# Kernel optimization log

Measured on AMD Instinct MI355X. Metric: run time of the kernel, lower is better.

The kernel has to match this reference:

```python
import jax, jax.numpy as jnp
import numpy as np

IN_CH = 128
OUT_CH = 1
N_NODES = 20000
N_EDGES = 640000
EPS = 1e-5


def setup_inputs() -> dict:
    key = jax.random.key(0)
    ks = jax.random.split(key, 8)
    x = jax.random.normal(ks[0], (N_NODES, IN_CH), dtype=jnp.float32)
    edge_index = jax.random.randint(ks[1], (2, N_EDGES), 0, N_NODES, dtype=jnp.int64)
    s1 = 1.0 / np.sqrt(2 * IN_CH)
    s2 = 1.0 / np.sqrt(IN_CH)
    return {
        "x": x,
        "edge_index": edge_index,
        "W1": jax.random.normal(ks[2], (2 * IN_CH, IN_CH), dtype=jnp.float32) * s1,
        "b1": jnp.zeros((IN_CH,), dtype=jnp.float32),
        "bn_g": jnp.ones((IN_CH,), dtype=jnp.float32),
        "bn_b": jnp.zeros((IN_CH,), dtype=jnp.float32),
        "W2": jax.random.normal(ks[3], (IN_CH, IN_CH), dtype=jnp.float32) * s2,
        "b2": jnp.zeros((IN_CH,), dtype=jnp.float32),
        "ln_g": jnp.ones((IN_CH,), dtype=jnp.float32),
        "ln_b": jnp.zeros((IN_CH,), dtype=jnp.float32),
        "W3": jax.random.normal(ks[4], (IN_CH, OUT_CH), dtype=jnp.float32) * s2,
        "b3": jnp.zeros((OUT_CH,), dtype=jnp.float32),
    }


def gcn_conv(h, src, dst, num_nodes, bias):
    # h: [num_nodes, F] already linearly transformed. GCN norm with self loops:
    # deg[i] = 1 + in-degree(i); norm_e = deg[src]^-1/2 * deg[dst]^-1/2
    deg = jnp.zeros((num_nodes,), h.dtype).at[dst].add(1.0) + 1.0
    dinv = deg ** -0.5
    norm = dinv[src] * dinv[dst]                      # [E]
    agg = jnp.zeros_like(h).at[dst].add(h[src] * norm[:, None])
    agg = agg + h * (dinv * dinv)[:, None]            # self-loop contribution
    return agg + bias


def reference(x, edge_index, W1, b1, bn_g, bn_b, W2, b2, ln_g, ln_b, W3, b3):
    src, dst = edge_index[0], edge_index[1]
    E = src.shape[0]
    # edge features: [E, 2*IN_CH]
    ef = jnp.concatenate([x[src], x[dst]], axis=1)
    # GCNConv 1 over E "nodes" (edge-feature rows)
    h = gcn_conv(ef @ W1, src, dst, E, b1)
    # BatchNorm1d (training-mode batch stats, biased variance)
    mean = h.mean(axis=0)
    var = h.var(axis=0)
    h = (h - mean) * jax.lax.rsqrt(var + EPS) * bn_g + bn_b
    h = jax.nn.relu(h)
    # GCNConv 2
    h = gcn_conv(h @ W2, src, dst, E, b2)
    # LayerNorm over feature dim
    mu = h.mean(axis=-1, keepdims=True)
    v = h.var(axis=-1, keepdims=True)
    h = (h - mu) * jax.lax.rsqrt(v + EPS) * ln_g + ln_b
    h = jax.nn.relu(h)
    out = h @ W3 + b3                                  # [E, 1]
    return out.squeeze()
```

## Files before the change

### kernel.cpp

```cpp
#include <hip/hip_runtime.h>
#include <hip/hip_bf16.h>

#define NN 20000
#define NE 640000
#define TAILN (NE - NN)
#define F  128
#define EPSN 1e-5f

typedef __bf16 bf16;
typedef bf16  bf16x8 __attribute__((ext_vector_type(8)));
typedef bf16  bf16x4 __attribute__((ext_vector_type(4)));
typedef float f32x4  __attribute__((ext_vector_type(4)));
typedef float f32x2  __attribute__((ext_vector_type(2)));
typedef unsigned short u16;

__global__ void k_cvt_idx(const void* __restrict__ ei_raw, int* __restrict__ srcb,
                          int* __restrict__ dstb, int* __restrict__ cnt,
                          int* __restrict__ cst, int* __restrict__ cdt) {
  const int* e32 = (const int*)ei_raw;
  const long long* e64 = (const long long*)ei_raw;
  bool is64 = true;
#pragma unroll
  for (int k = 0; k < 8; ++k) is64 = is64 && (e32[2 * k + 1] == 0);
  int e = blockIdx.x * 256 + threadIdx.x;
  if (e < NE) {
    int s, d;
    if (is64) { s = (int)e64[e]; d = (int)e64[NE + e]; }
    else      { s = e32[e];      d = e32[NE + e]; }
    srcb[e] = s; dstb[e] = d;
    atomicAdd(&cnt[d], 1);
    if (e >= NN) { atomicAdd(&cst[s], 1); atomicAdd(&cdt[d], 1); }
  }
}

__global__ __launch_bounds__(256) void k1_gemm1(const float* __restrict__ x,
        const float* __restrict__ W1, bf16* __restrict__ xa, bf16* __restrict__ xb) {
  __shared__ float XT[64][129];
  int row0 = blockIdx.x * 64;
  int half = blockIdx.y >> 1;
  int cb   = (blockIdx.y & 1) * 64;
  const float* W = W1 + (size_t)half * F * F;
  bf16* out = half ? xb : xa;
  int t = threadIdx.x;
#pragma unroll
  for (int i = 0; i < 8; ++i) {
    int flat = i * 1024 + t * 4;
    int r = flat >> 7, c = flat & 127;
    int gr = row0 + r;
    f32x4 v = {0.f, 0.f, 0.f, 0.f};
    if (gr < NN) v = *(const f32x4*)(x + (size_t)gr * F + c);
    XT[r][c] = v[0]; XT[r][c + 1] = v[1]; XT[r][c + 2] = v[2]; XT[r][c + 3] = v[3];
  }
  __syncthreads();
  int tc = t & 15, tr = t >> 4;
  float acc[4][4] = {};
  for (int k = 0; k < F; ++k) {
    f32x4 wv = *(const f32x4*)(W + (size_t)k * F + cb + tc * 4);
    float x0 = XT[tr * 4 + 0][k], x1 = XT[tr * 4 + 1][k];
    float x2 = XT[tr * 4 + 2][k], x3 = XT[tr * 4 + 3][k];
#pragma unroll
    for (int j = 0; j < 4; ++j) {
      acc[0][j] += x0 * wv[j]; acc[1][j] += x1 * wv[j];
      acc[2][j] += x2 * wv[j]; acc[3][j] += x3 * wv[j];
    }
  }
#pragma unroll
  for (int i = 0; i < 4; ++i) {
    int gr = row0 + tr * 4 + i;
    if (gr < NN) {
      bf16x4 o;
#pragma unroll
      for (int j = 0; j < 4; ++j) o[j] = (bf16)acc[i][j];
      *(bf16x4*)(out + (size_t)gr * F + cb + tc * 4) = o;
    }
  }
}

__global__ __launch_bounds__(1024) void k3_scan(const int* __restrict__ cnt,
        int* __restrict__ ptr, int* __restrict__ cursor,
        float* __restrict__ dinv, float* __restrict__ invdeg) {
  __shared__ int wsum[16];
  __shared__ int carry_s;
  int t = threadIdx.x;
  int lane = t & 63, wv = t >> 6;
  if (t == 0) carry_s = 0;
  __syncthreads();
  for (int c0 = 0; c0 < NN; c0 += 1024) {
    int i = c0 + t;
    int v = (i < NN) ? cnt[i] : 0;
    int s = v;
#pragma unroll
    for (int off = 1; off < 64; off <<= 1) {
      int n = __shfl_up(s, off);
      if (lane >= off) s += n;
    }
    if (lane == 63) wsum[wv] = s;
    __syncthreads();
    int carry = carry_s;
    int wbase = 0;
#pragma unroll
    for (int k2 = 0; k2 < 16; ++k2) wbase += (k2 < wv) ? wsum[k2] : 0;
    int incl = s + wbase;
    if (i < NN) {
      int excl = carry + incl - v;
      ptr[i] = excl; cursor[i] = excl;
      float deg = (float)(v + 1);
      dinv[i] = rsqrtf(deg);
      invdeg[i] = 1.0f / deg;
    }
    __syncthreads();
    if (t == 1023) carry_s = carry + incl;
    __syncthreads();
  }
  if (t == 0) ptr[NN] = carry_s;
}

__global__ void k4_hhead(const int* __restrict__ srcb, const int* __restrict__ dstb,
                         const bf16* __restrict__ xa, const bf16* __restrict__ xb,
                         bf16* __restrict__ hh) {
  int flat = blockIdx.x * 256 + threadIdx.x;
  int j = flat >> 4, ch = flat & 15;
  if (j >= NN) return;
  int s = srcb[j], d = dstb[j];
  bf16x8 a = *(const bf16x8*)(xa + (size_t)s * F + ch * 8);
  bf16x8 b = *(const bf16x8*)(xb + (size_t)d * F + ch * 8);
  bf16x8 o;
#pragma unroll
  for (int m = 0; m < 8; ++m) o[m] = (bf16)((float)a[m] + (float)b[m]);
  *(bf16x8*)(hh + (size_t)j * F + ch * 8) = o;
}

__global__ void k5_fill(const int* __restrict__ srcb, const int* __restrict__ dstb,
                        int* __restrict__ cursor, int* __restrict__ csr_s) {
  int e = blockIdx.x * 256 + threadIdx.x;
  if (e < NE) {
    int d = dstb[e];
    int pos = atomicAdd(&cursor[d], 1);
    csr_s[pos] = srcb[e] | ((e >= NN) ? (1 << 16) : 0);
  }
}

__global__ __launch_bounds__(256) void k6_conv1cross(const int* __restrict__ ptr,
        const int* __restrict__ csr_s, const bf16* __restrict__ hh,
        const bf16* __restrict__ xa, const bf16* __restrict__ xb,
        const float* __restrict__ dinv, const float* __restrict__ invdeg,
        const float* __restrict__ b1, float* __restrict__ h1h,
        float* __restrict__ crossrow) {
  int w = threadIdx.x >> 6, lane = threadIdx.x & 63;
  int g = lane >> 4, k = lane & 15;
  int i = blockIdx.x * 4 + w;
  int c0 = k * 8;
  int beg = ptr[i], end = ptr[i + 1];
  float acc[8] = {0,0,0,0,0,0,0,0}, z[8] = {0,0,0,0,0,0,0,0};
  int q = beg + g;
  for (; q + 4 < end; q += 8) {
    int v0 = csr_s[q], v1 = csr_s[q + 4];
    int s0 = v0 & 0xFFFF, s1 = v1 & 0xFFFF;
    float f0 = (v0 >> 16) ? 1.f : 0.f, f1 = (v1 >> 16) ? 1.f : 0.f;
    float d0 = dinv[s0], d1 = dinv[s1];
    bf16x8 h0 = *(const bf16x8*)(hh + (size_t)s0 * F + c0);
    bf16x8 x0 = *(const bf16x8*)(xa + (size_t)s0 * F + c0);
    bf16x8 h1 = *(const bf16x8*)(hh + (size_t)s1 * F + c0);
    bf16x8 x1 = *(const bf16x8*)(xa + (size_t)s1 * F + c0);
#pragma unroll
    for (int j = 0; j < 8; ++j) {
      acc[j] += d0 * (float)h0[j] + d1 * (float)h1[j];
      z[j]   += f0 * (float)x0[j] + f1 * (float)x1[j];
    }
  }
  if (q < end) {
    int v0 = csr_s[q];
    int s0 = v0 & 0xFFFF;
    float f0 = (v0 >> 16) ? 1.f : 0.f;
    float d0 = dinv[s0];
    bf16x8 h0 = *(const bf16x8*)(hh + (size_t)s0 * F + c0);
    bf16x8 x0 = *(const bf16x8*)(xa + (size_t)s0 * F + c0);
#pragma unroll
    for (int j = 0; j < 8; ++j) {
      acc[j] += d0 * (float)h0[j];
      z[j]   += f0 * (float)x0[j];
    }
  }
#pragma unroll
  for (int m = 16; m < 64; m <<= 1) {
#pragma unroll
    for (int j = 0; j < 8; ++j) {
      acc[j] += __shfl_xor(acc[j], m);
      z[j]   += __shfl_xor(z[j], m);
    }
  }
  if (g == 0) {
    float di = dinv[i], iv = invdeg[i];
    bf16x8 self = *(const bf16x8*)(hh + (size_t)i * F + c0);
    f32x4 bA = *(const f32x4*)(b1 + c0), bB = *(const f32x4*)(b1 + c0 + 4);
    f32x4 o0, o1;
#pragma unroll
    for (int j = 0; j < 4; ++j) {
      o0[j] = di * acc[j]     + (float)self[j]     * iv + bA[j];
      o1[j] = di * acc[j + 4] + (float)self[j + 4] * iv + bB[j];
    }
    *(f32x4*)(h1h + (size_t)i * F + c0) = o0;
    *(f32x4*)(h1h + (size_t)i * F + c0 + 4) = o1;
  } else if (g == 1) {
    bf16x8 xbv = *(const bf16x8*)(xb + (size_t)i * F + c0);
    f32x4 o0, o1;
#pragma unroll
    for (int j = 0; j < 4; ++j) {
      o0[j] = (float)xbv[j]     * z[j];
      o1[j] = (float)xbv[j + 4] * z[j + 4];
    }
    *(f32x4*)(crossrow + (size_t)i * F + c0) = o0;
    *(f32x4*)(crossrow + (size_t)i * F + c0 + 4) = o1;
  }
}

__global__ __launch_bounds__(256) void k7sr(const float* __restrict__ h1h,
        const float* __restrict__ crossrow, const bf16* __restrict__ xa,
        const bf16* __restrict__ xb, const int* __restrict__ cst,
        const int* __restrict__ cdt, float* __restrict__ statsB) {
  int t = threadIdx.x;
  int w = t >> 6, lane = t & 63, k = lane & 15;
  int rg = t >> 4;
  int c0 = k * 8;
  int base = blockIdx.x * 200;
  float A1[8] = {0,0,0,0,0,0,0,0}, A2[8] = {0,0,0,0,0,0,0,0};
  float B1[8] = {0,0,0,0,0,0,0,0}, B2[8] = {0,0,0,0,0,0,0,0};
  float Cc[8] = {0,0,0,0,0,0,0,0};
  for (int r = rg; r < 200; r += 16) {
    int n = base + r;
    f32x4 h0 = *(const f32x4*)(h1h + (size_t)n * F + c0);
    f32x4 h1 = *(const f32x4*)(h1h + (size_t)n * F + c0 + 4);
    f32x4 cr0 = *(const f32x4*)(crossrow + (size_t)n * F + c0);
    f32x4 cr1 = *(const f32x4*)(crossrow + (size_t)n * F + c0 + 4);
    bf16x8 av = *(const bf16x8*)(xa + (size_t)n * F + c0);
    bf16x8 bv = *(const bf16x8*)(xb + (size_t)n * F + c0);
    float ca = (float)cst[n], cb = (float)cdt[n];
#pragma unroll
    for (int j = 0; j < 4; ++j) {
      A1[j] += h0[j]; A2[j] += h0[j] * h0[j];
      A1[j + 4] += h1[j]; A2[j + 4] += h1[j] * h1[j];
      Cc[j] += cr0[j]; Cc[j + 4] += cr1[j];
    }
#pragma unroll
    for (int j = 0; j < 8; ++j) {
      float a = (float)av[j], b = (float)bv[j];
      B1[j] += ca * a + cb * b;
      B2[j] += ca * a * a + cb * b * b;
    }
  }
#pragma unroll
  for (int m = 16; m < 64; m <<= 1) {
#pragma unroll
    for (int j = 0; j < 8; ++j) {
      A1[j] += __shfl_xor(A1[j], m); A2[j] += __shfl_xor(A2[j], m);
      B1[j] += __shfl_xor(B1[j], m); B2[j] += __shfl_xor(B2[j], m);
      Cc[j] += __shfl_xor(Cc[j], m);
    }
  }
  __shared__ float L[4][5][128];
  if (lane < 16) {
#pragma unroll
    for (int j = 0; j < 8; ++j) {
      L[w][0][c0 + j] = A1[j]; L[w][1][c0 + j] = A2[j];
      L[w][2][c0 + j] = B1[j]; L[w][3][c0 + j] = B2[j];
      L[w][4][c0 + j] = Cc[j];
    }
  }
  __syncthreads();
  if (t < 128) {
#pragma unroll
    for (int term = 0; term < 5; ++term) {
      float v = L[0][term][t] + L[1][term][t] + L[2][term][t] + L[3][term][t];
      atomicAdd(&statsB[term * 128 + t], v);
    }
  }
}

__global__ __launch_bounds__(256) void k8_final(const float* __restrict__ statsB,
        const float* __restrict__ bn_g, const float* __restrict__ bn_b,
        const float* __restrict__ b1, const float* __restrict__ W2,
        const float* __restrict__ b2, const float* __restrict__ lng,
        const float* __restrict__ lnb, const float* __restrict__ W3,
        float* __restrict__ P, float* __restrict__ Qh, float* __restrict__ Qt,
        u16* __restrict__ W2t, f32x4* __restrict__ params4) {
  int t = threadIdx.x;
  if (t < 128) {
    float A1 = statsB[t], A2 = statsB[128 + t], B1v = statsB[256 + t];
    float B2v = statsB[384 + t], Cv = statsB[512 + t];
    float b1c = b1[t];
    float S = A1 + B1v + (float)TAILN * b1c;
    float Q = A2 + B2v + 2.f * Cv + 2.f * b1c * B1v + (float)TAILN * b1c * b1c;
    float mean = S * (1.0f / NE);
    float var = Q * (1.0f / NE) - mean * mean;
    float rs = rsqrtf(var + EPSN);
    float p = bn_g[t] * rs;
    float sh = bn_b[t] - mean * p;
    P[t] = p; Qh[t] = sh; Qt[t] = p * b1c + sh;
    f32x4 pr = {b2[t], lng[t], lnb[t], W3[t]};
    params4[t] = pr;
  }
  for (int i = 0; i < 64; ++i) {
    int flat = i * 256 + t;
    int k = flat >> 7, c = flat & 127;
    union { bf16 b; u16 u; } cv;
    cv.b = (bf16)W2[(size_t)k * F + c];
    W2t[(size_t)c * F + k] = cv.u;
  }
}

__global__ __launch_bounds__(256) void k9a_headgemm(const float* __restrict__ h1h,
        const float* __restrict__ P, const float* __restrict__ Qh,
        const u16* __restrict__ W2t, bf16* __restrict__ h2ph) {
  __shared__ __align__(16) bf16 A[64 * 128];
  __shared__ __align__(16) bf16 B[128 * 128];
  int t = threadIdx.x;
  int row0 = blockIdx.x * 64;
  const bf16x8* srcB = (const bf16x8*)W2t;
#pragma unroll
  for (int i = 0; i < 8; ++i) {
    int ch = i * 256 + t;
    int r = ch >> 4, cir = ch & 15;
    *(bf16x8*)&B[r * 128 + ((cir ^ (r & 7)) << 3)] = srcB[ch];
  }
  {
    int r = t >> 2, sub = t & 3;
    int gr = row0 + r;
#pragma unroll
    for (int j = 0; j < 4; ++j) {
      int c0 = sub * 32 + j * 8;
      f32x4 v0 = {0.f,0.f,0.f,0.f}, v1 = {0.f,0.f,0.f,0.f};
      if (gr < NN) {
        v0 = *(const f32x4*)(h1h + (size_t)gr * F + c0);
        v1 = *(const f32x4*)(h1h + (size_t)gr * F + c0 + 4);
      }
      f32x4 p0 = *(const f32x4*)(P + c0), p1 = *(const f32x4*)(P + c0 + 4);
      f32x4 q0 = *(const f32x4*)(Qh + c0), q1 = *(const f32x4*)(Qh + c0 + 4);
      bf16x8 o;
#pragma unroll
      for (int m = 0; m < 4; ++m) {
        o[m]     = (bf16)fmaxf(v0[m] * p0[m] + q0[m], 0.f);
        o[m + 4] = (bf16)fmaxf(v1[m] * p1[m] + q1[m], 0.f);
      }
      int ch = c0 >> 3;
      *(bf16x8*)&A[r * 128 + ((ch ^ (r & 7)) << 3)] = o;
    }
  }
  __syncthreads();
  int lane = t & 63, w = t >> 6;
  int lr = lane & 15, g = lane >> 4;
  int arow = w * 16 + lr;
  bf16x8 af[4];
#pragma unroll
  for (int kk = 0; kk < 4; ++kk)
    af[kk] = *(const bf16x8*)&A[arow * 128 + (((kk * 4 + g) ^ (arow & 7)) << 3)];
  f32x4 acc[8];
#pragma unroll
  for (int n = 0; n < 8; ++n) {
    f32x4 a = {0.f,0.f,0.f,0.f};
    int col = n * 16 + lr;
#pragma unroll
    for (int kk = 0; kk < 4; ++kk) {
      bf16x8 bfr = *(const bf16x8*)&B[col * 128 + (((kk * 4 + g) ^ (col & 7)) << 3)];
      a = __builtin_amdgcn_mfma_f32_16x16x32_bf16(af[kk], bfr, a, 0, 0, 0);
    }
    acc[n] = a;
  }
#pragma unroll
  for (int n = 0; n < 8; ++n) {
#pragma unroll
    for (int r4 = 0; r4 < 4; ++r4) {
      int gr = row0 + w * 16 + g * 4 + r4;
      if (gr < NN) h2ph[(size_t)gr * F + n * 16 + lr] = (bf16)acc[n][r4];
    }
  }
}

__global__ __launch_bounds__(256) void k9b_head(const int* __restrict__ ptr,
        const int* __restrict__ csr_s, const bf16* __restrict__ h2ph,
        const float* __restrict__ dinv, const float* __restrict__ invdeg,
        const float* __restrict__ b2, const float* __restrict__ lng,
        const float* __restrict__ lnb, const float* __restrict__ W3,
        const float* __restrict__ b3, float* __restrict__ out) {
  int w = threadIdx.x >> 6, lane = threadIdx.x & 63;
  int g = lane >> 4, k = lane & 15;
  int i = blockIdx.x * 4 + w;
  int c0 = k * 8;
  int beg = ptr[i], end = ptr[i + 1];
  float acc[8] = {0,0,0,0,0,0,0,0};
  int q = beg + g;
  for (; q + 4 < end; q += 8) {
    int s0 = csr_s[q] & 0xFFFF, s1 = csr_s[q + 4] & 0xFFFF;
    float d0 = dinv[s0], d1 = dinv[s1];
    bf16x8 h0 = *(const bf16x8*)(h2ph + (size_t)s0 * F + c0);
    bf16x8 h1 = *(const bf16x8*)(h2ph + (size_t)s1 * F + c0);
#pragma unroll
    for (int j = 0; j < 8; ++j)
      acc[j] += d0 * (float)h0[j] + d1 * (float)h1[j];
  }
  if (q < end) {
    int s0 = csr_s[q] & 0xFFFF;
    float d0 = dinv[s0];
    bf16x8 h0 = *(const bf16x8*)(h2ph + (size_t)s0 * F + c0);
#pragma unroll
    for (int j = 0; j < 8; ++j) acc[j] += d0 * (float)h0[j];
  }
#pragma unroll
  for (int m = 16; m < 64; m <<= 1) {
#pragma unroll
    for (int j = 0; j < 8; ++j) acc[j] += __shfl_xor(acc[j], m);
  }
  float di = dinv[i], iv = invdeg[i];
  bf16x8 self = *(const bf16x8*)(h2ph + (size_t)i * F + c0);
  f32x4 b2A = *(const f32x4*)(b2 + c0), b2B = *(const f32x4*)(b2 + c0 + 4);
  float h2[8];
#pragma unroll
  for (int j = 0; j < 4; ++j) {
    h2[j]     = di * acc[j]     + (float)self[j]     * iv + b2A[j];
    h2[j + 4] = di * acc[j + 4] + (float)self[j + 4] * iv + b2B[j];
  }
  float s1v = 0.f, s2v = 0.f;
#pragma unroll
  for (int j = 0; j < 8; ++j) { s1v += h2[j]; s2v += h2[j] * h2[j]; }
#pragma unroll
  for (int m = 1; m < 16; m <<= 1) { s1v += __shfl_xor(s1v, m); s2v += __shfl_xor(s2v, m); }
  float mean = s1v * (1.0f / F);
  float var = s2v * (1.0f / F) - mean * mean;
  float rs = rsqrtf(var + EPSN);
  f32x4 lgA = *(const f32x4*)(lng + c0), lgB = *(const f32x4*)(lng + c0 + 4);
  f32x4 lbA = *(const f32x4*)(lnb + c0), lbB = *(const f32x4*)(lnb + c0 + 4);
  f32x4 w3A = *(const f32x4*)(W3 + c0),  w3B = *(const f32x4*)(W3 + c0 + 4);
  float y = 0.f;
#pragma unroll
  for (int j = 0; j < 4; ++j) {
    y += fmaxf((h2[j]     - mean) * rs * lgA[j] + lbA[j], 0.f) * w3A[j];
    y += fmaxf((h2[j + 4] - mean) * rs * lgB[j] + lbB[j], 0.f) * w3B[j];
  }
#pragma unroll
  for (int m = 1; m < 16; m <<= 1) y += __shfl_xor(y, m);
  if (lane == 0) out[i] = y + b3[0];
}

__global__ __launch_bounds__(256) void k9c_tail(const int* __restrict__ srcb,
        const int* __restrict__ dstb, const bf16* __restrict__ xa,
        const bf16* __restrict__ xb, const float* __restrict__ P,
        const float* __restrict__ Qt, const u16* __restrict__ W2t,
        const f32x4* __restrict__ params4, const float* __restrict__ b3,
        float* __restrict__ out) {
  __shared__ __align__(16) bf16 B[128 * 128];
  int t = threadIdx.x;
  const bf16x8* srcB = (const bf16x8*)W2t;
#pragma unroll
  for (int i = 0; i < 8; ++i) {
    int ch = i * 256 + t;
    int r = ch >> 4, cir = ch & 15;
    *(bf16x8*)&B[r * 128 + ((cir ^ (r & 7)) << 3)] = srcB[ch];
  }
  __syncthreads();
  int lane = t & 63, w = t >> 6;
  int lr = lane & 15, g = lane >> 4;
  int ebase = NN + blockIdx.x * 256 + w * 64;
  float b3v = b3[0];
  for (int rc = 0; rc < 4; ++rc) {
    int e = ebase + rc * 16 + lr;
    bool ok = (e < NE);
    int se = 0, de = 0;
    if (ok) { se = srcb[e]; de = dstb[e]; }
    bf16x8 af[4];
#pragma unroll
    for (int kk = 0; kk < 4; ++kk) {
      int c0 = kk * 32 + g * 8;
      bf16x8 o;
      if (ok) {
        bf16x8 av = *(const bf16x8*)(xa + (size_t)se * F + c0);
        bf16x8 bv = *(const bf16x8*)(xb + (size_t)de * F + c0);
        f32x4 p0 = *(const f32x4*)(P + c0), p1 = *(const f32x4*)(P + c0 + 4);
        f32x4 q0 = *(const f32x4*)(Qt + c0), q1 = *(const f32x4*)(Qt + c0 + 4);
#pragma unroll
        for (int m = 0; m < 4; ++m) {
          o[m]     = (bf16)fmaxf(((float)av[m] + (float)bv[m]) * p0[m] + q0[m], 0.f);
          o[m + 4] = (bf16)fmaxf(((float)av[m + 4] + (float)bv[m + 4]) * p1[m] + q1[m], 0.f);
        }
      } else {
#pragma unroll
        for (int m = 0; m < 8; ++m) o[m] = (bf16)0.f;
      }
      af[kk] = o;
    }
    f32x4 acc[8];
#pragma unroll
    for (int n = 0; n < 8; ++n) {
      f32x4 a = {0.f,0.f,0.f,0.f};
      int col = n * 16 + lr;
#pragma unroll
      for (int kk = 0; kk < 4; ++kk) {
        bf16x8 bfr = *(const bf16x8*)&B[col * 128 + (((kk * 4 + g) ^ (col & 7)) << 3)];
        a = __builtin_amdgcn_mfma_f32_16x16x32_bf16(af[kk], bfr, a, 0, 0, 0);
      }
      acc[n] = a;
    }
#pragma unroll
    for (int r4 = 0; r4 < 4; ++r4) {
      float vv[8];
      float s = 0.f, q = 0.f;
#pragma unroll
      for (int n = 0; n < 8; ++n) {
        float v = acc[n][r4] + params4[n * 16 + lr][0];
        vv[n] = v; s += v; q += v * v;
      }
#pragma unroll
      for (int m = 1; m < 16; m <<= 1) { s += __shfl_xor(s, m); q += __shfl_xor(q, m); }
      float mean = s * (1.0f / F);
      float var = q * (1.0f / F) - mean * mean;
      float rs = rsqrtf(var + EPSN);
      float o = 0.f;
#pragma unroll
      for (int n = 0; n < 8; ++n) {
        f32x4 pr = params4[n * 16 + lr];
        o += fmaxf((vv[n] - mean) * rs * pr[1] + pr[2], 0.f) * pr[3];
      }
#pragma unroll
      for (int m = 1; m < 16; m <<= 1) o += __shfl_xor(o, m);
      int eo = ebase + rc * 16 + g * 4 + r4;
      if (lr == 0 && eo < NE) out[eo] = o + b3v;
    }
  }
}

extern "C" void kernel_launch(void* const* d_in, const int* in_sizes, int n_in,
                              void* d_out, int out_size, void* d_ws, size_t ws_size,
                              hipStream_t stream) {
  const float* x   = (const float*)d_in[0];
  const void*  ei  = d_in[1];
  const float* W1  = (const float*)d_in[2];
  const float* b1  = (const float*)d_in[3];
  const float* bng = (const float*)d_in[4];
  const float* bnb = (const float*)d_in[5];
  const float* W2  = (const float*)d_in[6];
  const float* b2  = (const float*)d_in[7];
  const float* lng = (const float*)d_in[8];
  const float* lnb = (const float*)d_in[9];
  const float* W3  = (const float*)d_in[10];
  const float* b3  = (const float*)d_in[11];
  float* out = (float*)d_out;

  char* ws = (char*)d_ws;
  size_t off = 0;
  auto alloc = [&](size_t bytes) -> char* {
    off = (off + 511) & ~(size_t)511;
    char* p = ws + off;
    off += bytes;
    return p;
  };
  const size_t NFh = (size_t)NN * F * 2;
  bf16*  xa     = (bf16*)alloc(NFh);
  bf16*  xb     = (bf16*)alloc(NFh);
  bf16*  hh     = (bf16*)alloc(NFh);
  float* h1h    = (float*)alloc((size_t)NN * F * 4);
  float* crossr = (float*)alloc((size_t)NN * F * 4);
  int*   srcb   = (int*)alloc((size_t)NE * 4);
  int*   dstb   = (int*)alloc((size_t)NE * 4);
  int*   csr_s  = (int*)alloc((size_t)NE * 4);
  int*   cnt    = (int*)alloc((size_t)NN * 4);
  int*   cst    = (int*)alloc((size_t)NN * 4);
  int*   cdt    = (int*)alloc((size_t)NN * 4);
  int*   ptrb   = (int*)alloc((size_t)(NN + 1) * 4);
  int*   cursor = (int*)alloc((size_t)NN * 4);
  float* dinv   = (float*)alloc((size_t)NN * 4);
  float* invdeg = (float*)alloc((size_t)NN * 4);
  float* statsB = (float*)alloc(5 * 128 * 4);
  float* Pp     = (float*)alloc(128 * 4);
  float* Qh     = (float*)alloc(128 * 4);
  float* Qt     = (float*)alloc(128 * 4);
  u16*   W2t    = (u16*)alloc((size_t)F * F * 2);
  f32x4* params4= (f32x4*)alloc(128 * 16);
  bf16*  h2ph   = hh;

  hipMemsetAsync(cnt, 0, (size_t)NN * 4, stream);
  hipMemsetAsync(cst, 0, (size_t)NN * 4, stream);
  hipMemsetAsync(cdt, 0, (size_t)NN * 4, stream);
  hipMemsetAsync(statsB, 0, 5 * 128 * 4, stream);

  k_cvt_idx<<<2500, 256, 0, stream>>>(ei, srcb, dstb, cnt, cst, cdt);
  k1_gemm1<<<dim3(313, 4), 256, 0, stream>>>(x, W1, xa, xb);
  k3_scan<<<1, 1024, 0, stream>>>(cnt, ptrb, cursor, dinv, invdeg);
  k4_hhead<<<1250, 256, 0, stream>>>(srcb, dstb, xa, xb, hh);
  k5_fill<<<2500, 256, 0, stream>>>(srcb, dstb, cursor, csr_s);
  k6_conv1cross<<<5000, 256, 0, stream>>>(ptrb, csr_s, hh, xa, xb, dinv, invdeg, b1,
                                          h1h, crossr);
  k7sr<<<100, 256, 0, stream>>>(h1h, crossr, xa, xb, cst, cdt, statsB);
  k8_final<<<1, 256, 0, stream>>>(statsB, bng, bnb, b1, W2, b2, lng, lnb, W3,
                                  Pp, Qh, Qt, W2t, params4);
  k9a_headgemm<<<313, 256, 0, stream>>>(h1h, Pp, Qh, W2t, h2ph);
  k9b_head<<<5000, 256, 0, stream>>>(ptrb, csr_s, h2ph, dinv, invdeg, b2, lng, lnb,
                                     W3, b3, out);
  k9c_tail<<<2422, 256, 0, stream>>>(srcb, dstb, xa, xb, Pp, Qt, W2t, params4,
                                     b3, out);
}
```

Baseline: 461.0 us.

## Merge independent kernels into block-range fused launches to cut launch count

Independent kernels are merged into single launches that branch on block index: index conversion with the first GEMM and W2 transpose/param packing, head-sum with CSR fill, and the head and tail output kernels. The W2 transpose moves out of the single-block k8 into the first fused kernel, leaving k8 as a 128-thread stats finalize. This removes several launch gaps and tail-drain serialisation between kernels. In exchange the fused kernels carry the larger shared-memory footprint and register pressure of their heaviest branch, which can lower occupancy for the light branches, especially the 32KB LDS tile in kC applied to head blocks.

```diff
diff --git a/kernel.cpp b/kernel.cpp
--- a/kernel.cpp
+++ b/kernel.cpp
@@ -11,67 +11,86 @@
 typedef bf16  bf16x8 __attribute__((ext_vector_type(8)));
 typedef bf16  bf16x4 __attribute__((ext_vector_type(4)));
 typedef float f32x4  __attribute__((ext_vector_type(4)));
-typedef float f32x2  __attribute__((ext_vector_type(2)));
 typedef unsigned short u16;
 
-__global__ void k_cvt_idx(const void* __restrict__ ei_raw, int* __restrict__ srcb,
-                          int* __restrict__ dstb, int* __restrict__ cnt,
-                          int* __restrict__ cst, int* __restrict__ cdt) {
-  const int* e32 = (const int*)ei_raw;
-  const long long* e64 = (const long long*)ei_raw;
-  bool is64 = true;
-#pragma unroll
-  for (int k = 0; k < 8; ++k) is64 = is64 && (e32[2 * k + 1] == 0);
-  int e = blockIdx.x * 256 + threadIdx.x;
-  if (e < NE) {
-    int s, d;
-    if (is64) { s = (int)e64[e]; d = (int)e64[NE + e]; }
-    else      { s = e32[e];      d = e32[NE + e]; }
-    srcb[e] = s; dstb[e] = d;
-    atomicAdd(&cnt[d], 1);
-    if (e >= NN) { atomicAdd(&cst[s], 1); atomicAdd(&cdt[d], 1); }
-  }
-}
-
-__global__ __launch_bounds__(256) void k1_gemm1(const float* __restrict__ x,
-        const float* __restrict__ W1, bf16* __restrict__ xa, bf16* __restrict__ xb) {
+__global__ __launch_bounds__(256) void kA_fused(const void* __restrict__ ei_raw,
+        int* __restrict__ srcb, int* __restrict__ dstb, int* __restrict__ cnt,
+        int* __restrict__ cst, int* __restrict__ cdt,
+        const float* __restrict__ x, const float* __restrict__ W1,
+        bf16* __restrict__ xa, bf16* __restrict__ xb,
+        const float* __restrict__ W2, const float* __restrict__ b2,
+        const float* __restrict__ lng, const float* __restrict__ lnb,
+        const float* __restrict__ W3, u16* __restrict__ W2t,
+        f32x4* __restrict__ params4) {
   __shared__ float XT[64][129];
-  int row0 = blockIdx.x * 64;
-  int half = blockIdx.y >> 1;
-  int cb   = (blockIdx.y & 1) * 64;
-  const float* W = W1 + (size_t)half * F * F;
-  bf16* out = half ? xb : xa;
+  int bid = blockIdx.x;
   int t = threadIdx.x;
-#pragma unroll
-  for (int i = 0; i < 8; ++i) {
-    int flat = i * 1024 + t * 4;
-    int r = flat >> 7, c = flat & 127;
-    int gr = row0 + r;
-    f32x4 v = {0.f, 0.f, 0.f, 0.f};
-    if (gr < NN) v = *(const f32x4*)(x + (size_t)gr * F + c);
-    XT[r][c] = v[0]; XT[r][c + 1] = v[1]; XT[r][c + 2] = v[2]; XT[r][c + 3] = v[3];
-  }
-  __syncthreads();
-  int tc = t & 15, tr = t >> 4;
-  float acc[4][4] = {};
-  for (int k = 0; k < F; ++k) {
-    f32x4 wv = *(const f32x4*)(W + (size_t)k * F + cb + tc * 4);
-    float x0 = XT[tr * 4 + 0][k], x1 = XT[tr * 4 + 1][k];
-    float x2 = XT[tr * 4 + 2][k], x3 = XT[tr * 4 + 3][k];
-#pragma unroll
-    for (int j = 0; j < 4; ++j) {
-      acc[0][j] += x0 * wv[j]; acc[1][j] += x1 * wv[j];
-      acc[2][j] += x2 * wv[j]; acc[3][j] += x3 * wv[j];
-    }
-  }
-#pragma unroll
-  for (int i = 0; i < 4; ++i) {
-    int gr = row0 + tr * 4 + i;
-    if (gr < NN) {
-      bf16x4 o;
-#pragma unroll
-      for (int j = 0; j < 4; ++j) o[j] = (bf16)acc[i][j];
-      *(bf16x4*)(out + (size_t)gr * F + cb + tc * 4) = o;
+  if (bid < 2500) {
+    const int* e32 = (const int*)ei_raw;
+    const long long* e64 = (const long long*)ei_raw;
+    bool is64 = true;
+#pragma unroll
+    for (int k = 0; k < 8; ++k) is64 = is64 && (e32[2 * k + 1] == 0);
+    int e = bid * 256 + t;
+    if (e < NE) {
+      int s, d;
+      if (is64) { s = (int)e64[e]; d = (int)e64[NE + e]; }
+      else      { s = e32[e];      d = e32[NE + e]; }
+      srcb[e] = s; dstb[e] = d;
+      atomicAdd(&cnt[d], 1);
+      if (e >= NN) { atomicAdd(&cst[s], 1); atomicAdd(&cdt[d], 1); }
+    }
+  } else if (bid < 3752) {
+    int idx = bid - 2500;
+    int row0 = (idx >> 2) * 64;
+    int by = idx & 3;
+    int half = by >> 1;
+    int cb = (by & 1) * 64;
+    const float* W = W1 + (size_t)half * F * F;
+    bf16* out = half ? xb : xa;
+#pragma unroll
+    for (int i = 0; i < 8; ++i) {
+      int flat = i * 1024 + t * 4;
+      int r = flat >> 7, c = flat & 127;
+      int gr = row0 + r;
+      f32x4 v = {0.f, 0.f, 0.f, 0.f};
+      if (gr < NN) v = *(const f32x4*)(x + (size_t)gr * F + c);
+      XT[r][c] = v[0]; XT[r][c + 1] = v[1]; XT[r][c + 2] = v[2]; XT[r][c + 3] = v[3];
+    }
+    __syncthreads();
+    int tc = t & 15, tr = t >> 4;
+    float acc[4][4] = {};
+    for (int k = 0; k < F; ++k) {
+      f32x4 wv = *(const f32x4*)(W + (size_t)k * F + cb + tc * 4);
+      float x0 = XT[tr * 4 + 0][k], x1 = XT[tr * 4 + 1][k];
+      float x2 = XT[tr * 4 + 2][k], x3 = XT[tr * 4 + 3][k];
+#pragma unroll
+      for (int j = 0; j < 4; ++j) {
+        acc[0][j] += x0 * wv[j]; acc[1][j] += x1 * wv[j];
+        acc[2][j] += x2 * wv[j]; acc[3][j] += x3 * wv[j];
+      }
+    }
+#pragma unroll
+    for (int i = 0; i < 4; ++i) {
+      int gr = row0 + tr * 4 + i;
+      if (gr < NN) {
+        bf16x4 o;
+#pragma unroll
+        for (int j = 0; j < 4; ++j) o[j] = (bf16)acc[i][j];
+        *(bf16x4*)(out + (size_t)gr * F + cb + tc * 4) = o;
+      }
+    }
+  } else {
+    if (t < 128) {
+      f32x4 pr = {b2[t], lng[t], lnb[t], W3[t]};
+      params4[t] = pr;
+    }
+    for (int i = 0; i < 64; ++i) {
+      int flat = i * 256 + t;
+      int k = flat >> 7, c = flat & 127;
+      union { bf16 b; u16 u; } cv;
+      cv.b = (bf16)W2[(size_t)k * F + c];
+      W2t[(size_t)c * F + k] = cv.u;
     }
   }
 }
@@ -115,28 +134,30 @@
   if (t == 0) ptr[NN] = carry_s;
 }
 
-__global__ void k4_hhead(const int* __restrict__ srcb, const int* __restrict__ dstb,
-                         const bf16* __restrict__ xa, const bf16* __restrict__ xb,
-                         bf16* __restrict__ hh) {
-  int flat = blockIdx.x * 256 + threadIdx.x;
-  int j = flat >> 4, ch = flat & 15;
-  if (j >= NN) return;
-  int s = srcb[j], d = dstb[j];
-  bf16x8 a = *(const bf16x8*)(xa + (size_t)s * F + ch * 8);
-  bf16x8 b = *(const bf16x8*)(xb + (size_t)d * F + ch * 8);
-  bf16x8 o;
-#pragma unroll
-  for (int m = 0; m < 8; ++m) o[m] = (bf16)((float)a[m] + (float)b[m]);
-  *(bf16x8*)(hh + (size_t)j * F + ch * 8) = o;
-}
-
-__global__ void k5_fill(const int* __restrict__ srcb, const int* __restrict__ dstb,
-                        int* __restrict__ cursor, int* __restrict__ csr_s) {
-  int e = blockIdx.x * 256 + threadIdx.x;
-  if (e < NE) {
-    int d = dstb[e];
-    int pos = atomicAdd(&cursor[d], 1);
-    csr_s[pos] = srcb[e] | ((e >= NN) ? (1 << 16) : 0);
+__global__ __launch_bounds__(256) void kB_fused(const int* __restrict__ srcb,
+        const int* __restrict__ dstb, const bf16* __restrict__ xa,
+        const bf16* __restrict__ xb, bf16* __restrict__ hh,
+        int* __restrict__ cursor, int* __restrict__ csr_s) {
+  int bid = blockIdx.x;
+  int t = threadIdx.x;
+  if (bid < 1250) {
+    int flat = bid * 256 + t;
+    int j = flat >> 4, ch = flat & 15;
+    if (j >= NN) return;
+    int s = srcb[j], d = dstb[j];
+    bf16x8 a = *(const bf16x8*)(xa + (size_t)s * F + ch * 8);
+    bf16x8 b = *(const bf16x8*)(xb + (size_t)d * F + ch * 8);
+    bf16x8 o;
+#pragma unroll
+    for (int m = 0; m < 8; ++m) o[m] = (bf16)((float)a[m] + (float)b[m]);
+    *(bf16x8*)(hh + (size_t)j * F + ch * 8) = o;
+  } else {
+    int e = (bid - 1250) * 256 + t;
+    if (e < NE) {
+      int d = dstb[e];
+      int pos = atomicAdd(&cursor[d], 1);
+      csr_s[pos] = srcb[e] | ((e >= NN) ? (1 << 16) : 0);
+    }
   }
 }
 
@@ -276,36 +297,22 @@
   }
 }
 
-__global__ __launch_bounds__(256) void k8_final(const float* __restrict__ statsB,
+__global__ __launch_bounds__(128) void k8_small(const float* __restrict__ statsB,
         const float* __restrict__ bn_g, const float* __restrict__ bn_b,
-        const float* __restrict__ b1, const float* __restrict__ W2,
-        const float* __restrict__ b2, const float* __restrict__ lng,
-        const float* __restrict__ lnb, const float* __restrict__ W3,
-        float* __restrict__ P, float* __restrict__ Qh, float* __restrict__ Qt,
-        u16* __restrict__ W2t, f32x4* __restrict__ params4) {
+        const float* __restrict__ b1,
+        float* __restrict__ P, float* __restrict__ Qh, float* __restrict__ Qt) {
   int t = threadIdx.x;
-  if (t < 128) {
-    float A1 = statsB[t], A2 = statsB[128 + t], B1v = statsB[256 + t];
-    float B2v = statsB[384 + t], Cv = statsB[512 + t];
-    float b1c = b1[t];
-    float S = A1 + B1v + (float)TAILN * b1c;
-    float Q = A2 + B2v + 2.f * Cv + 2.f * b1c * B1v + (float)TAILN * b1c * b1c;
-    float mean = S * (1.0f / NE);
-    float var = Q * (1.0f / NE) - mean * mean;
-    float rs = rsqrtf(var + EPSN);
-    float p = bn_g[t] * rs;
-    float sh = bn_b[t] - mean * p;
-    P[t] = p; Qh[t] = sh; Qt[t] = p * b1c + sh;
-    f32x4 pr = {b2[t], lng[t], lnb[t], W3[t]};
-    params4[t] = pr;
-  }
-  for (int i = 0; i < 64; ++i) {
-    int flat = i * 256 + t;
-    int k = flat >> 7, c = flat & 127;
-    union { bf16 b; u16 u; } cv;
-    cv.b = (bf16)W2[(size_t)k * F + c];
-    W2t[(size_t)c * F + k] = cv.u;
-  }
+  float A1 = statsB[t], A2 = statsB[128 + t], B1v = statsB[256 + t];
+  float B2v = statsB[384 + t], Cv = statsB[512 + t];
+  float b1c = b1[t];
+  float S = A1 + B1v + (float)TAILN * b1c;
+  float Q = A2 + B2v + 2.f * Cv + 2.f * b1c * B1v + (float)TAILN * b1c * b1c;
+  float mean = S * (1.0f / NE);
+  float var = Q * (1.0f / NE) - mean * mean;
+  float rs = rsqrtf(var + EPSN);
+  float p = bn_g[t] * rs;
+  float sh = bn_b[t] - mean * p;
+  P[t] = p; Qh[t] = sh; Qt[t] = p * b1c + sh;
 }
 
 __global__ __launch_bounds__(256) void k9a_headgemm(const float* __restrict__ h1h,
@@ -375,153 +382,153 @@
   }
 }
 
-__global__ __launch_bounds__(256) void k9b_head(const int* __restrict__ ptr,
+__global__ __launch_bounds__(256) void kC_fused(const int* __restrict__ ptr,
         const int* __restrict__ csr_s, const bf16* __restrict__ h2ph,
         const float* __restrict__ dinv, const float* __restrict__ invdeg,
         const float* __restrict__ b2, const float* __restrict__ lng,
         const float* __restrict__ lnb, const float* __restrict__ W3,
-        const float* __restrict__ b3, float* __restrict__ out) {
-  int w = threadIdx.x >> 6, lane = threadIdx.x & 63;
-  int g = lane >> 4, k = lane & 15;
-  int i = blockIdx.x * 4 + w;
-  int c0 = k * 8;
-  int beg = ptr[i], end = ptr[i + 1];
-  float acc[8] = {0,0,0,0,0,0,0,0};
-  int q = beg + g;
-  for (; q + 4 < end; q += 8) {
-    int s0 = csr_s[q] & 0xFFFF, s1 = csr_s[q + 4] & 0xFFFF;
-    float d0 = dinv[s0], d1 = dinv[s1];
-    bf16x8 h0 = *(const bf16x8*)(h2ph + (size_t)s0 * F + c0);
-    bf16x8 h1 = *(const bf16x8*)(h2ph + (size_t)s1 * F + c0);
-#pragma unroll
-    for (int j = 0; j < 8; ++j)
-      acc[j] += d0 * (float)h0[j] + d1 * (float)h1[j];
-  }
-  if (q < end) {
-    int s0 = csr_s[q] & 0xFFFF;
-    float d0 = dinv[s0];
-    bf16x8 h0 = *(const bf16x8*)(h2ph + (size_t)s0 * F + c0);
-#pragma unroll
-    for (int j = 0; j < 8; ++j) acc[j] += d0 * (float)h0[j];
-  }
-#pragma unroll
-  for (int m = 16; m < 64; m <<= 1) {
-#pragma unroll
-    for (int j = 0; j < 8; ++j) acc[j] += __shfl_xor(acc[j], m);
-  }
-  float di = dinv[i], iv = invdeg[i];
-  bf16x8 self = *(const bf16x8*)(h2ph + (size_t)i * F + c0);
-  f32x4 b2A = *(const f32x4*)(b2 + c0), b2B = *(const f32x4*)(b2 + c0 + 4);
-  float h2[8];
-#pragma unroll
-  for (int j = 0; j < 4; ++j) {
-    h2[j]     = di * acc[j]     + (float)self[j]     * iv + b2A[j];
-    h2[j + 4] = di * acc[j + 4] + (float)self[j + 4] * iv + b2B[j];
-  }
-  float s1v = 0.f, s2v = 0.f;
-#pragma unroll
-  for (int j = 0; j < 8; ++j) { s1v += h2[j]; s2v += h2[j] * h2[j]; }
-#pragma unroll
-  for (int m = 1; m < 16; m <<= 1) { s1v += __shfl_xor(s1v, m); s2v += __shfl_xor(s2v, m); }
-  float mean = s1v * (1.0f / F);
-  float var = s2v * (1.0f / F) - mean * mean;
-  float rs = rsqrtf(var + EPSN);
-  f32x4 lgA = *(const f32x4*)(lng + c0), lgB = *(const f32x4*)(lng + c0 + 4);
-  f32x4 lbA = *(const f32x4*)(lnb + c0), lbB = *(const f32x4*)(lnb + c0 + 4);
-  f32x4 w3A = *(const f32x4*)(W3 + c0),  w3B = *(const f32x4*)(W3 + c0 + 4);
-  float y = 0.f;
-#pragma unroll
-  for (int j = 0; j < 4; ++j) {
-    y += fmaxf((h2[j]     - mean) * rs * lgA[j] + lbA[j], 0.f) * w3A[j];
-    y += fmaxf((h2[j + 4] - mean) * rs * lgB[j] + lbB[j], 0.f) * w3B[j];
-  }
-#pragma unroll
-  for (int m = 1; m < 16; m <<= 1) y += __shfl_xor(y, m);
-  if (lane == 0) out[i] = y + b3[0];
-}
-
-__global__ __launch_bounds__(256) void k9c_tail(const int* __restrict__ srcb,
-        const int* __restrict__ dstb, const bf16* __restrict__ xa,
-        const bf16* __restrict__ xb, const float* __restrict__ P,
-        const float* __restrict__ Qt, const u16* __restrict__ W2t,
-        const f32x4* __restrict__ params4, const float* __restrict__ b3,
-        float* __restrict__ out) {
+        const float* __restrict__ b3, float* __restrict__ out,
+        const int* __restrict__ srcb, const int* __restrict__ dstb,
+        const bf16* __restrict__ xa, const bf16* __restrict__ xb,
+        const float* __restrict__ P, const float* __restrict__ Qt,
+        const u16* __restrict__ W2t, const f32x4* __restrict__ params4) {
   __shared__ __align__(16) bf16 B[128 * 128];
+  int bid = blockIdx.x;
   int t = threadIdx.x;
-  const bf16x8* srcB = (const bf16x8*)W2t;
-#pragma unroll
-  for (int i = 0; i < 8; ++i) {
-    int ch = i * 256 + t;
-    int r = ch >> 4, cir = ch & 15;
-    *(bf16x8*)&B[r * 128 + ((cir ^ (r & 7)) << 3)] = srcB[ch];
-  }
-  __syncthreads();
   int lane = t & 63, w = t >> 6;
-  int lr = lane & 15, g = lane >> 4;
-  int ebase = NN + blockIdx.x * 256 + w * 64;
-  float b3v = b3[0];
-  for (int rc = 0; rc < 4; ++rc) {
-    int e = ebase + rc * 16 + lr;
-    bool ok = (e < NE);
-    int se = 0, de = 0;
-    if (ok) { se = srcb[e]; de = dstb[e]; }
-    bf16x8 af[4];
-#pragma unroll
-    for (int kk = 0; kk < 4; ++kk) {
-      int c0 = kk * 32 + g * 8;
-      bf16x8 o;
-      if (ok) {
-        bf16x8 av = *(const bf16x8*)(xa + (size_t)se * F + c0);
-        bf16x8 bv = *(const bf16x8*)(xb + (size_t)de * F + c0);
-        f32x4 p0 = *(const f32x4*)(P + c0), p1 = *(const f32x4*)(P + c0 + 4);
-        f32x4 q0 = *(const f32x4*)(Qt + c0), q1 = *(const f32x4*)(Qt + c0 + 4);
-#pragma unroll
-        for (int m = 0; m < 4; ++m) {
-          o[m]     = (bf16)fmaxf(((float)av[m] + (float)bv[m]) * p0[m] + q0[m], 0.f);
-          o[m + 4] = (bf16)fmaxf(((float)av[m + 4] + (float)bv[m + 4]) * p1[m] + q1[m], 0.f);
+  if (bid < 5000) {
+    int g = lane >> 4, k = lane & 15;
+    int i = bid * 4 + w;
+    int c0 = k * 8;
+    int beg = ptr[i], end = ptr[i + 1];
+    float acc[8] = {0,0,0,0,0,0,0,0};
+    int q = beg + g;
+    for (; q + 4 < end; q += 8) {
+      int s0 = csr_s[q] & 0xFFFF, s1 = csr_s[q + 4] & 0xFFFF;
+      float d0 = dinv[s0], d1 = dinv[s1];
+      bf16x8 h0 = *(const bf16x8*)(h2ph + (size_t)s0 * F + c0);
+      bf16x8 h1 = *(const bf16x8*)(h2ph + (size_t)s1 * F + c0);
+#pragma unroll
+      for (int j = 0; j < 8; ++j)
+        acc[j] += d0 * (float)h0[j] + d1 * (float)h1[j];
+    }
+    if (q < end) {
+      int s0 = csr_s[q] & 0xFFFF;
+      float d0 = dinv[s0];
+      bf16x8 h0 = *(const bf16x8*)(h2ph + (size_t)s0 * F + c0);
+#pragma unroll
+      for (int j = 0; j < 8; ++j) acc[j] += d0 * (float)h0[j];
+    }
+#pragma unroll
+    for (int m = 16; m < 64; m <<= 1) {
+#pragma unroll
+      for (int j = 0; j < 8; ++j) acc[j] += __shfl_xor(acc[j], m);
+    }
+    float di = dinv[i], iv = invdeg[i];
+    bf16x8 self = *(const bf16x8*)(h2ph + (size_t)i * F + c0);
+    f32x4 b2A = *(const f32x4*)(b2 + c0), b2B = *(const f32x4*)(b2 + c0 + 4);
+    float h2[8];
+#pragma unroll
+    for (int j = 0; j < 4; ++j) {
+      h2[j]     = di * acc[j]     + (float)self[j]     * iv + b2A[j];
+      h2[j + 4] = di * acc[j + 4] + (float)self[j + 4] * iv + b2B[j];
+    }
+    float s1v = 0.f, s2v = 0.f;
+#pragma unroll
+    for (int j = 0; j < 8; ++j) { s1v += h2[j]; s2v += h2[j] * h2[j]; }
+#pragma unroll
+    for (int m = 1; m < 16; m <<= 1) { s1v += __shfl_xor(s1v, m); s2v += __shfl_xor(s2v, m); }
+    float mean = s1v * (1.0f / F);
+    float var = s2v * (1.0f / F) - mean * mean;
+    float rs = rsqrtf(var + EPSN);
+    f32x4 lgA = *(const f32x4*)(lng + c0), lgB = *(const f32x4*)(lng + c0 + 4);
+    f32x4 lbA = *(const f32x4*)(lnb + c0), lbB = *(const f32x4*)(lnb + c0 + 4);
+    f32x4 w3A = *(const f32x4*)(W3 + c0),  w3B = *(const f32x4*)(W3 + c0 + 4);
+    float y = 0.f;
+#pragma unroll
+    for (int j = 0; j < 4; ++j) {
+      y += fmaxf((h2[j]     - mean) * rs * lgA[j] + lbA[j], 0.f) * w3A[j];
+      y += fmaxf((h2[j + 4] - mean) * rs * lgB[j] + lbB[j], 0.f) * w3B[j];
+    }
+#pragma unroll
+    for (int m = 1; m < 16; m <<= 1) y += __shfl_xor(y, m);
+    if (lane == 0) out[i] = y + b3[0];
+  } else {
+    int bid2 = bid - 5000;
+    const bf16x8* srcB = (const bf16x8*)W2t;
+#pragma unroll
+    for (int i = 0; i < 8; ++i) {
+      int ch = i * 256 + t;
+      int r = ch >> 4, cir = ch & 15;
+      *(bf16x8*)&B[r * 128 + ((cir ^ (r & 7)) << 3)] = srcB[ch];
+    }
+    __syncthreads();
+    int lr = lane & 15, g = lane >> 4;
+    int ebase = NN + bid2 * 256 + w * 64;
+    float b3v = b3[0];
+    for (int rc = 0; rc < 4; ++rc) {
+      int e = ebase + rc * 16 + lr;
+      bool ok = (e < NE);
+      int se = 0, de = 0;
+      if (ok) { se = srcb[e]; de = dstb[e]; }
+      bf16x8 af[4];
+#pragma unroll
+      for (int kk = 0; kk < 4; ++kk) {
+        int c0 = kk * 32 + g * 8;
+        bf16x8 o;
+        if (ok) {
+          bf16x8 av = *(const bf16x8*)(xa + (size_t)se * F + c0);
+          bf16x8 bv = *(const bf16x8*)(xb + (size_t)de * F + c0);
+          f32x4 p0 = *(const f32x4*)(P + c0), p1 = *(const f32x4*)(P + c0 + 4);
+          f32x4 q0 = *(const f32x4*)(Qt + c0), q1 = *(const f32x4*)(Qt + c0 + 4);
+#pragma unroll
+          for (int m = 0; m < 4; ++m) {
+            o[m]     = (bf16)fmaxf(((float)av[m] + (float)bv[m]) * p0[m] + q0[m], 0.f);
+            o[m + 4] = (bf16)fmaxf(((float)av[m + 4] + (float)bv[m + 4]) * p1[m] + q1[m], 0.f);
+          }
+        } else {
+#pragma unroll
+          for (int m = 0; m < 8; ++m) o[m] = (bf16)0.f;
         }
-      } else {
-#pragma unroll
-        for (int m = 0; m < 8; ++m) o[m] = (bf16)0.f;
+        af[kk] = o;
       }
-      af[kk] = o;
-    }
-    f32x4 acc[8];
-#pragma unroll
-    for (int n = 0; n < 8; ++n) {
-      f32x4 a = {0.f,0.f,0.f,0.f};
-      int col = n * 16 + lr;
-#pragma unroll
-      for (int kk = 0; kk < 4; ++kk) {
-        bf16x8 bfr = *(const bf16x8*)&B[col * 128 + (((kk * 4 + g) ^ (col & 7)) << 3)];
-        a = __builtin_amdgcn_mfma_f32_16x16x32_bf16(af[kk], bfr, a, 0, 0, 0);
+      f32x4 acc[8];
+#pragma unroll
+      for (int n = 0; n < 8; ++n) {
+        f32x4 a = {0.f,0.f,0.f,0.f};
+        int col = n * 16 + lr;
+#pragma unroll
+        for (int kk = 0; kk < 4; ++kk) {
+          bf16x8 bfr = *(const bf16x8*)&B[col * 128 + (((kk * 4 + g) ^ (col & 7)) << 3)];
+          a = __builtin_amdgcn_mfma_f32_16x16x32_bf16(af[kk], bfr, a, 0, 0, 0);
+        }
+        acc[n] = a;
       }
-      acc[n] = a;
-    }
-#pragma unroll
-    for (int r4 = 0; r4 < 4; ++r4) {
-      float vv[8];
-      float s = 0.f, q = 0.f;
-#pragma unroll
-      for (int n = 0; n < 8; ++n) {
-        float v = acc[n][r4] + params4[n * 16 + lr][0];
-        vv[n] = v; s += v; q += v * v;
+#pragma unroll
+      for (int r4 = 0; r4 < 4; ++r4) {
+        float vv[8];
+        float s = 0.f, q = 0.f;
+#pragma unroll
+        for (int n = 0; n < 8; ++n) {
+          float v = acc[n][r4] + params4[n * 16 + lr][0];
+          vv[n] = v; s += v; q += v * v;
+        }
+#pragma unroll
+        for (int m = 1; m < 16; m <<= 1) { s += __shfl_xor(s, m); q += __shfl_xor(q, m); }
+        float mean = s * (1.0f / F);
+        float var = q * (1.0f / F) - mean * mean;
+        float rs = rsqrtf(var + EPSN);
+        float o = 0.f;
+#pragma unroll
+        for (int n = 0; n < 8; ++n) {
+          f32x4 pr = params4[n * 16 + lr];
+          o += fmaxf((vv[n] - mean) * rs * pr[1] + pr[2], 0.f) * pr[3];
+        }
+#pragma unroll
+        for (int m = 1; m < 16; m <<= 1) o += __shfl_xor(o, m);
+        int eo = ebase + rc * 16 + g * 4 + r4;
+        if (lr == 0 && eo < NE) out[eo] = o + b3v;
       }
-#pragma unroll
-      for (int m = 1; m < 16; m <<= 1) { s += __shfl_xor(s, m); q += __shfl_xor(q, m); }
-      float mean = s * (1.0f / F);
-      float var = q * (1.0f / F) - mean * mean;
-      float rs = rsqrtf(var + EPSN);
-      float o = 0.f;
-#pragma unroll
-      for (int n = 0; n < 8; ++n) {
-        f32x4 pr = params4[n * 16 + lr];
-        o += fmaxf((vv[n] - mean) * rs * pr[1] + pr[2], 0.f) * pr[3];
-      }
-#pragma unroll
-      for (int m = 1; m < 16; m <<= 1) o += __shfl_xor(o, m);
-      int eo = ebase + rc * 16 + g * 4 + r4;
-      if (lr == 0 && eo < NE) out[eo] = o + b3v;
     }
   }
 }
@@ -580,19 +587,16 @@
   hipMemsetAsync(cdt, 0, (size_t)NN * 4, stream);
   hipMemsetAsync(statsB, 0, 5 * 128 * 4, stream);
 
-  k_cvt_idx<<<2500, 256, 0, stream>>>(ei, srcb, dstb, cnt, cst, cdt);
-  k1_gemm1<<<dim3(313, 4), 256, 0, stream>>>(x, W1, xa, xb);
+  kA_fused<<<3753, 256, 0, stream>>>(ei, srcb, dstb, cnt, cst, cdt, x, W1, xa, xb,
+                                     W2, b2, lng, lnb, W3, W2t, params4);
   k3_scan<<<1, 1024, 0, stream>>>(cnt, ptrb, cursor, dinv, invdeg);
-  k4_hhead<<<1250, 256, 0, stream>>>(srcb, dstb, xa, xb, hh);
-  k5_fill<<<2500, 256, 0, stream>>>(srcb, dstb, cursor, csr_s);
+  kB_fused<<<3750, 256, 0, stream>>>(srcb, dstb, xa, xb, hh, cursor, csr_s);
   k6_conv1cross<<<5000, 256, 0, stream>>>(ptrb, csr_s, hh, xa, xb, dinv, invdeg, b1,
                                           h1h, crossr);
   k7sr<<<100, 256, 0, stream>>>(h1h, crossr, xa, xb, cst, cdt, statsB);
-  k8_final<<<1, 256, 0, stream>>>(statsB, bng, bnb, b1, W2, b2, lng, lnb, W3,
-                                  Pp, Qh, Qt, W2t, params4);
+  k8_small<<<1, 128, 0, stream>>>(statsB, bng, bnb, b1, Pp, Qh, Qt);
   k9a_headgemm<<<313, 256, 0, stream>>>(h1h, Pp, Qh, W2t, h2ph);
-  k9b_head<<<5000, 256, 0, stream>>>(ptrb, csr_s, h2ph, dinv, invdeg, b2, lng, lnb,
-                                     W3, b3, out);
-  k9c_tail<<<2422, 256, 0, stream>>>(srcb, dstb, xa, xb, Pp, Qt, W2t, params4,
-                                     b3, out);
-}
+  kC_fused<<<7422, 256, 0, stream>>>(ptrb, csr_s, h2ph, dinv, invdeg, b2, lng, lnb,
+                                     W3, b3, out, srcb, dstb, xa, xb, Pp, Qt, W2t,
+                                     params4);
+}
```

Result: slower. 581.5 us (+26.1%).

## Fuse head-build and CSR fill kernels; interleave hh and xa rows for gather

Applied to the files above, without the earlier changes.

Merges the head-row construction and CSR fill into one launch using block-index ranges, and writes an interleaved buffer where each row holds the hh values followed by a copy of the xa row. The conv1 gather then reads both vectors from one 512-byte row instead of two separate arrays, which is meant to improve locality of the random gathers. It costs an extra copy of xa into the interleaved buffer and one fewer kernel launch. h2ph now aliases the larger buffer.

```diff
diff --git a/kernel.cpp b/kernel.cpp
--- a/kernel.cpp
+++ b/kernel.cpp
@@ -11,7 +11,6 @@
 typedef bf16  bf16x8 __attribute__((ext_vector_type(8)));
 typedef bf16  bf16x4 __attribute__((ext_vector_type(4)));
 typedef float f32x4  __attribute__((ext_vector_type(4)));
-typedef float f32x2  __attribute__((ext_vector_type(2)));
 typedef unsigned short u16;
 
 __global__ void k_cvt_idx(const void* __restrict__ ei_raw, int* __restrict__ srcb,
@@ -115,34 +114,42 @@
   if (t == 0) ptr[NN] = carry_s;
 }
 
-__global__ void k4_hhead(const int* __restrict__ srcb, const int* __restrict__ dstb,
-                         const bf16* __restrict__ xa, const bf16* __restrict__ xb,
-                         bf16* __restrict__ hh) {
-  int flat = blockIdx.x * 256 + threadIdx.x;
-  int j = flat >> 4, ch = flat & 15;
-  if (j >= NN) return;
-  int s = srcb[j], d = dstb[j];
-  bf16x8 a = *(const bf16x8*)(xa + (size_t)s * F + ch * 8);
-  bf16x8 b = *(const bf16x8*)(xb + (size_t)d * F + ch * 8);
-  bf16x8 o;
-#pragma unroll
-  for (int m = 0; m < 8; ++m) o[m] = (bf16)((float)a[m] + (float)b[m]);
-  *(bf16x8*)(hh + (size_t)j * F + ch * 8) = o;
-}
-
-__global__ void k5_fill(const int* __restrict__ srcb, const int* __restrict__ dstb,
-                        int* __restrict__ cursor, int* __restrict__ csr_s) {
-  int e = blockIdx.x * 256 + threadIdx.x;
-  if (e < NE) {
-    int d = dstb[e];
-    int pos = atomicAdd(&cursor[d], 1);
-    csr_s[pos] = srcb[e] | ((e >= NN) ? (1 << 16) : 0);
+__global__ __launch_bounds__(256) void kB_fused(const int* __restrict__ srcb,
+        const int* __restrict__ dstb, const bf16* __restrict__ xa,
+        const bf16* __restrict__ xb, bf16* __restrict__ hx,
+        int* __restrict__ cursor, int* __restrict__ csr_s) {
+  int bid = blockIdx.x;
+  int t = threadIdx.x;
+  if (bid < 2500) {
+    int flat = bid * 256 + t;
+    int j = flat >> 5, ch = flat & 31;
+    if (j >= NN) return;
+    if (ch < 16) {
+      int s = srcb[j], d = dstb[j];
+      bf16x8 a = *(const bf16x8*)(xa + (size_t)s * F + ch * 8);
+      bf16x8 b = *(const bf16x8*)(xb + (size_t)d * F + ch * 8);
+      bf16x8 o;
+#pragma unroll
+      for (int m = 0; m < 8; ++m) o[m] = (bf16)((float)a[m] + (float)b[m]);
+      *(bf16x8*)(hx + (size_t)j * 256 + ch * 8) = o;
+    } else {
+      int c8 = (ch - 16) * 8;
+      bf16x8 a = *(const bf16x8*)(xa + (size_t)j * F + c8);
+      *(bf16x8*)(hx + (size_t)j * 256 + 128 + c8) = a;
+    }
+  } else {
+    int e = (bid - 2500) * 256 + t;
+    if (e < NE) {
+      int d = dstb[e];
+      int pos = atomicAdd(&cursor[d], 1);
+      csr_s[pos] = srcb[e] | ((e >= NN) ? (1 << 16) : 0);
+    }
   }
 }
 
 __global__ __launch_bounds__(256) void k6_conv1cross(const int* __restrict__ ptr,
-        const int* __restrict__ csr_s, const bf16* __restrict__ hh,
-        const bf16* __restrict__ xa, const bf16* __restrict__ xb,
+        const int* __restrict__ csr_s, const bf16* __restrict__ hx,
+        const bf16* __restrict__ xb,
         const float* __restrict__ dinv, const float* __restrict__ invdeg,
         const float* __restrict__ b1, float* __restrict__ h1h,
         float* __restrict__ crossrow) {
@@ -158,10 +165,12 @@
     int s0 = v0 & 0xFFFF, s1 = v1 & 0xFFFF;
     float f0 = (v0 >> 16) ? 1.f : 0.f, f1 = (v1 >> 16) ? 1.f : 0.f;
     float d0 = dinv[s0], d1 = dinv[s1];
-    bf16x8 h0 = *(const bf16x8*)(hh + (size_t)s0 * F + c0);
-    bf16x8 x0 = *(const bf16x8*)(xa + (size_t)s0 * F + c0);
-    bf16x8 h1 = *(const bf16x8*)(hh + (size_t)s1 * F + c0);
-    bf16x8 x1 = *(const bf16x8*)(xa + (size_t)s1 * F + c0);
+    const bf16* r0 = hx + (size_t)s0 * 256 + c0;
+    const bf16* r1 = hx + (size_t)s1 * 256 + c0;
+    bf16x8 h0 = *(const bf16x8*)r0;
+    bf16x8 x0 = *(const bf16x8*)(r0 + 128);
+    bf16x8 h1 = *(const bf16x8*)r1;
+    bf16x8 x1 = *(const bf16x8*)(r1 + 128);
 #pragma unroll
     for (int j = 0; j < 8; ++j) {
       acc[j] += d0 * (float)h0[j] + d1 * (float)h1[j];
@@ -173,8 +182,9 @@
     int s0 = v0 & 0xFFFF;
     float f0 = (v0 >> 16) ? 1.f : 0.f;
     float d0 = dinv[s0];
-    bf16x8 h0 = *(const bf16x8*)(hh + (size_t)s0 * F + c0);
-    bf16x8 x0 = *(const bf16x8*)(xa + (size_t)s0 * F + c0);
+    const bf16* r0 = hx + (size_t)s0 * 256 + c0;
+    bf16x8 h0 = *(const bf16x8*)r0;
+    bf16x8 x0 = *(const bf16x8*)(r0 + 128);
 #pragma unroll
     for (int j = 0; j < 8; ++j) {
       acc[j] += d0 * (float)h0[j];
@@ -191,7 +201,7 @@
   }
   if (g == 0) {
     float di = dinv[i], iv = invdeg[i];
-    bf16x8 self = *(const bf16x8*)(hh + (size_t)i * F + c0);
+    bf16x8 self = *(const bf16x8*)(hx + (size_t)i * 256 + c0);
     f32x4 bA = *(const f32x4*)(b1 + c0), bB = *(const f32x4*)(b1 + c0 + 4);
     f32x4 o0, o1;
 #pragma unroll
@@ -554,7 +564,7 @@
   const size_t NFh = (size_t)NN * F * 2;
   bf16*  xa     = (bf16*)alloc(NFh);
   bf16*  xb     = (bf16*)alloc(NFh);
-  bf16*  hh     = (bf16*)alloc(NFh);
+  bf16*  hx     = (bf16*)alloc((size_t)NN * 256 * 2);
   float* h1h    = (float*)alloc((size_t)NN * F * 4);
   float* crossr = (float*)alloc((size_t)NN * F * 4);
   int*   srcb   = (int*)alloc((size_t)NE * 4);
@@ -573,7 +583,7 @@
   float* Qt     = (float*)alloc(128 * 4);
   u16*   W2t    = (u16*)alloc((size_t)F * F * 2);
   f32x4* params4= (f32x4*)alloc(128 * 16);
-  bf16*  h2ph   = hh;
+  bf16*  h2ph   = hx;
 
   hipMemsetAsync(cnt, 0, (size_t)NN * 4, stream);
   hipMemsetAsync(cst, 0, (size_t)NN * 4, stream);
@@ -583,9 +593,8 @@
   k_cvt_idx<<<2500, 256, 0, stream>>>(ei, srcb, dstb, cnt, cst, cdt);
   k1_gemm1<<<dim3(313, 4), 256, 0, stream>>>(x, W1, xa, xb);
   k3_scan<<<1, 1024, 0, stream>>>(cnt, ptrb, cursor, dinv, invdeg);
-  k4_hhead<<<1250, 256, 0, stream>>>(srcb, dstb, xa, xb, hh);
-  k5_fill<<<2500, 256, 0, stream>>>(srcb, dstb, cursor, csr_s);
-  k6_conv1cross<<<5000, 256, 0, stream>>>(ptrb, csr_s, hh, xa, xb, dinv, invdeg, b1,
+  kB_fused<<<5000, 256, 0, stream>>>(srcb, dstb, xa, xb, hx, cursor, csr_s);
+  k6_conv1cross<<<5000, 256, 0, stream>>>(ptrb, csr_s, hx, xb, dinv, invdeg, b1,
                                           h1h, crossr);
   k7sr<<<100, 256, 0, stream>>>(h1h, crossr, xa, xb, cst, cdt, statsB);
   k8_final<<<1, 256, 0, stream>>>(statsB, bng, bnb, b1, W2, b2, lng, lnb, W3,
```

Measured after the change: 459.5 us. Within noise of the previous version (-0.3%).
